# Kernel optimization log

Measured on AMD Instinct MI355X. Metric: run time of the kernel, lower is better.

## Reference

```python
import jax, jax.numpy as jnp
import numpy as np

N, E, H, L, G = 20000, 320000, 256, 7, 512
ATOM_V, BOND_V, OUT = 128, 8, 128
EPS = 1e-7      # GENConv eps added after ReLU on messages
BN_EPS = 1e-5   # BatchNorm1d default eps


def setup_inputs() -> dict:
    key = jax.random.key(0)
    ks = jax.random.split(key, 9)
    return {
        "node_feats": jax.random.randint(ks[0], (N, 9), 0, 100, dtype=jnp.int32),
        "edge_feats": jax.random.randint(ks[1], (E, 3), 0, 5, dtype=jnp.int32),
        "src": jax.random.randint(ks[2], (E,), 0, N, dtype=jnp.int32),
        "dst": jax.random.randint(ks[3], (E,), 0, N, dtype=jnp.int32),
        "graph_ids": jnp.sort(jax.random.randint(ks[4], (N,), 0, G, dtype=jnp.int32)),
        "atom_emb": 0.1 * jax.random.normal(ks[5], (9, ATOM_V, H), dtype=jnp.float32),
        "bond_emb": 0.1 * jax.random.normal(ks[6], (L, 3, BOND_V, H), dtype=jnp.float32),
        "bn_gamma": jnp.ones((L, H), jnp.float32),
        "bn_beta": jnp.zeros((L, H), jnp.float32),
        "mlp_w": (1.0 / np.sqrt(H)) * jax.random.normal(ks[7], (L, H, H), dtype=jnp.float32),
        "mlp_b": jnp.zeros((L, H), jnp.float32),
        "w_out": (1.0 / np.sqrt(H)) * jax.random.normal(ks[8], (H, OUT), dtype=jnp.float32),
        "b_out": jnp.zeros((OUT,), jnp.float32),
    }


def reference(node_feats, edge_feats, src, dst, graph_ids,
              atom_emb, bond_emb, bn_gamma, bn_beta, mlp_w, mlp_b, w_out, b_out):
    # AtomEncoder: sum of per-column embeddings -> [N, H]
    hv = atom_emb[jnp.arange(9)[None, :], node_feats].sum(axis=1)
    col3 = jnp.arange(3)[None, :]
    for l in range(L):
        # BatchNorm1d (training-mode batch stats) -> ReLU  (dropout p=0)
        mu = hv.mean(axis=0)
        var = hv.var(axis=0)
        h1 = (hv - mu) * jax.lax.rsqrt(var + BN_EPS) * bn_gamma[l] + bn_beta[l]
        h1 = jax.nn.relu(h1)
        # GENConv: BondEncoder embedding, message = relu(h_src + he) + eps
        he = bond_emb[l][col3, edge_feats].sum(axis=1)          # [E, H]
        m = jax.nn.relu(h1[src] + he) + EPS                     # [E, H]
        # edge softmax over incoming edges per destination node (beta = 1.0)
        mmax = jax.ops.segment_max(m, dst, num_segments=N)      # [N, H]
        ex = jnp.exp(m - mmax[dst])
        denom = jax.ops.segment_sum(ex, dst, num_segments=N)    # [N, H]
        a = ex / denom[dst]
        agg = jax.ops.segment_sum(m * a, dst, num_segments=N)   # [N, H]
        # MLP (mlp_layers=1 -> single Linear) + outer residual
        hv = (h1 + agg) @ mlp_w[l] + mlp_b[l] + hv
    # AvgPooling over nodes of each graph
    cnt = jax.ops.segment_sum(jnp.ones((N,), hv.dtype), graph_ids, num_segments=G)
    hg = jax.ops.segment_sum(hv, graph_ids, num_segments=G) / jnp.maximum(cnt, 1.0)[:, None]
    return hg @ w_out + b_out  # [G, OUT]
```

## Files before the change

kernel.cpp:

```cpp
#include <hip/hip_runtime.h>

#define N_NODES 20000
#define N_EDGES 320000
#define HD 256
#define NLAYERS 7
#define NGRAPH 512
#define NOUT 128
#define NTILES 625

typedef __attribute__((ext_vector_type(8))) short bf16x8;
typedef __attribute__((ext_vector_type(4))) int i32x4;
typedef __attribute__((ext_vector_type(4))) float f32x4;

__device__ __forceinline__ ushort f2bf(float f) {
    union { float f; unsigned u; } v;
    v.f = f;
    unsigned r = (v.u + 0x7FFFu + ((v.u >> 16) & 1u)) >> 16;
    return (ushort)r;
}
__device__ __forceinline__ float bf2f(ushort u) {
    union { unsigned u; float f; } v;
    v.u = (unsigned)u << 16;
    return v.f;
}
__device__ __forceinline__ float bflo(unsigned p) {
    union { unsigned u; float f; } v;
    v.u = p << 16;
    return v.f;
}
__device__ __forceinline__ float bfhi(unsigned p) {
    union { unsigned u; float f; } v;
    v.u = p & 0xffff0000u;
    return v.f;
}

__global__ __launch_bounds__(256) void hist_kernel(const int* __restrict__ dst, int* __restrict__ hist) {
    int e = blockIdx.x * 256 + threadIdx.x;
    if (e < N_EDGES) atomicAdd(&hist[dst[e]], 1);
}

__global__ __launch_bounds__(1024) void scan_kernel(const int* __restrict__ hist,
                                                    int* __restrict__ row_ptr,
                                                    int* __restrict__ cursor) {
    __shared__ int sums[1024];
    int t = threadIdx.x;
    const int CH = 20;
    int base = t * CH;
    int local[20];
    int s = 0;
#pragma unroll
    for (int i = 0; i < CH; i++) {
        int v = (base + i < N_NODES) ? hist[base + i] : 0;
        local[i] = s;
        s += v;
    }
    sums[t] = s;
    __syncthreads();
    for (int off = 1; off < 1024; off <<= 1) {
        int v = (t >= off) ? sums[t - off] : 0;
        __syncthreads();
        sums[t] += v;
        __syncthreads();
    }
    int offset = (t == 0) ? 0 : sums[t - 1];
#pragma unroll
    for (int i = 0; i < CH; i++) {
        int idx = base + i;
        if (idx < N_NODES) {
            int v = offset + local[i];
            row_ptr[idx] = v;
            cursor[idx] = v;
        }
    }
    if (t == 1023) row_ptr[N_NODES] = sums[1023];
}

__global__ __launch_bounds__(256) void scatter_kernel(const int* __restrict__ dst,
                                                      const int* __restrict__ src,
                                                      const int* __restrict__ ef,
                                                      int* __restrict__ cursor,
                                                      unsigned* __restrict__ pack_sorted) {
    int e = blockIdx.x * 256 + threadIdx.x;
    if (e < N_EDGES) {
        int d = dst[e];
        int p = atomicAdd(&cursor[d], 1);
        unsigned cb = (unsigned)(ef[e * 3] * 25 + ef[e * 3 + 1] * 5 + ef[e * 3 + 2]);
        pack_sorted[p] = (unsigned)src[e] | (cb << 15);
    }
}

__global__ __launch_bounds__(256) void hetab_kernel(const float* __restrict__ bond,
                                                    ushort* __restrict__ he) {
    int idx = blockIdx.x * 256 + threadIdx.x;
    if (idx >= NLAYERS * 125 * HD) return;
    int h = idx & (HD - 1);
    int rem = idx >> 8;
    int l = rem / 125;
    int c = rem - l * 125;
    int f0 = c / 25, f1 = (c / 5) % 5, f2 = c % 5;
    const float* b = bond + (size_t)l * 3 * 8 * HD;
    he[idx] = f2bf(b[(0 * 8 + f0) * HD + h] + b[(1 * 8 + f1) * HD + h] + b[(2 * 8 + f2) * HD + h]);
}

__global__ __launch_bounds__(256) void wt_kernel(const float* __restrict__ W,
                                                 ushort* __restrict__ Wt) {
    int b = blockIdx.x;
    int l = b >> 8;
    int n = b & 255;
    int k = threadIdx.x;
    float v = W[((size_t)l * HD + k) * HD + n];
    int ks = k >> 5, kg = (k >> 3) & 3, j = k & 7;
    Wt[(((size_t)l * 8 + ks) * 256 + n) * 32 + kg * 8 + j] = f2bf(v);
}

__global__ __launch_bounds__(256) void atom_kernel(const int* __restrict__ nf,
                                                   const float* __restrict__ emb,
                                                   float* __restrict__ hv,
                                                   float* __restrict__ stats0) {
    int c = threadIdx.x;
    int n0 = blockIdx.x * 32;
    float s1 = 0.f, s2 = 0.f;
    for (int i = 0; i < 32; i++) {
        int n = n0 + i;
        const int* f = nf + n * 9;
        float v = 0.f;
#pragma unroll
        for (int j = 0; j < 9; j++) v += emb[(j * 128 + f[j]) * HD + c];
        hv[(size_t)n * HD + c] = v;
        s1 += v;
        s2 += v * v;
    }
    atomicAdd(&stats0[c], s1);
    atomicAdd(&stats0[HD + c], s2);
}

__global__ __launch_bounds__(256) void bn_kernel(const float* __restrict__ hv,
                                                 const float* __restrict__ stats,
                                                 const float* __restrict__ gamma,
                                                 const float* __restrict__ beta,
                                                 ushort* __restrict__ h1) {
    int tid = blockIdx.x * 256 + threadIdx.x;
    int idx = tid * 8;
    int c = idx & (HD - 1);
    float4 f0 = *reinterpret_cast<const float4*>(hv + idx);
    float4 f1 = *reinterpret_cast<const float4*>(hv + idx + 4);
    float v[8] = {f0.x, f0.y, f0.z, f0.w, f1.x, f1.y, f1.z, f1.w};
    ushort o[8];
#pragma unroll
    for (int j = 0; j < 8; j++) {
        float mu = stats[c + j] * (1.0f / N_NODES);
        float var = stats[HD + c + j] * (1.0f / N_NODES) - mu * mu;
        float a = gamma[c + j] * rsqrtf(fmaxf(var, 0.f) + 1e-5f);
        float b = beta[c + j] - mu * a;
        o[j] = f2bf(fmaxf(fmaf(v[j], a, b), 0.f));
    }
    i32x4 pack;
    pack.x = (int)o[0] | ((int)o[1] << 16);
    pack.y = (int)o[2] | ((int)o[3] << 16);
    pack.z = (int)o[4] | ((int)o[5] << 16);
    pack.w = (int)o[6] | ((int)o[7] << 16);
    *reinterpret_cast<i32x4*>(h1 + idx) = pack;
}

__global__ __launch_bounds__(256) void edge_kernel(const ushort* __restrict__ h1,
                                                   ushort* __restrict__ xbf,
                                                   const int* __restrict__ row_ptr,
                                                   const unsigned* __restrict__ pack_sorted,
                                                   const ushort* __restrict__ hetab) {
    int wv = threadIdx.x >> 6;
    int lane = threadIdx.x & 63;
    int n = blockIdx.x * 4 + wv;
    int c4 = lane * 4;
    int e0 = row_ptr[n];
    int deg = row_ptr[n + 1] - e0;

    float S0 = 0.f, S1 = 0.f, S2 = 0.f, S3 = 0.f;
    float T0 = 0.f, T1 = 0.f, T2 = 0.f, T3 = 0.f;

#define GATHER(i, P)                                                                          \
    uint2 hs##i = *reinterpret_cast<const uint2*>(h1 + ((size_t)((P) & 0x7FFFu) << 8) + c4);  \
    uint2 hb##i = *reinterpret_cast<const uint2*>(hetab + (((P) >> 15) << 8) + c4);

#define EDGE_PROC(HS, HB)                                                  \
    {                                                                      \
        float m0 = fmaxf(bflo(HS.x) + bflo(HB.x), 0.f);                    \
        float m1 = fmaxf(bfhi(HS.x) + bfhi(HB.x), 0.f);                    \
        float m2 = fmaxf(bflo(HS.y) + bflo(HB.y), 0.f);                    \
        float m3 = fmaxf(bfhi(HS.y) + bfhi(HB.y), 0.f);                    \
        float x0 = __expf(m0), x1 = __expf(m1), x2 = __expf(m2), x3 = __expf(m3); \
        S0 += x0; T0 = fmaf(m0, x0, T0);                                   \
        S1 += x1; T1 = fmaf(m1, x1, T1);                                   \
        S2 += x2; T2 = fmaf(m2, x2, T2);                                   \
        S3 += x3; T3 = fmaf(m3, x3, T3);                                   \
    }

    for (int base = 0; base < deg; base += 64) {
        int cnt = min(64, deg - base);
        unsigned pk = (lane < cnt) ? pack_sorted[e0 + base + lane] : 0u;
        int j = 0;
        for (; j + 4 <= cnt; j += 4) {
            unsigned p0 = __shfl(pk, j + 0);
            unsigned p1 = __shfl(pk, j + 1);
            unsigned p2 = __shfl(pk, j + 2);
            unsigned p3 = __shfl(pk, j + 3);
            GATHER(0, p0) GATHER(1, p1) GATHER(2, p2) GATHER(3, p3)
            EDGE_PROC(hs0, hb0) EDGE_PROC(hs1, hb1) EDGE_PROC(hs2, hb2) EDGE_PROC(hs3, hb3)
        }
        for (; j < cnt; j++) {
            unsigned p0 = __shfl(pk, j);
            GATHER(0, p0)
            EDGE_PROC(hs0, hb0)
        }
    }
#undef EDGE_PROC
#undef GATHER

    float a0 = (S0 > 0.f) ? (T0 / S0 + 1e-7f) : 0.f;
    float a1 = (S1 > 0.f) ? (T1 / S1 + 1e-7f) : 0.f;
    float a2 = (S2 > 0.f) ? (T2 / S2 + 1e-7f) : 0.f;
    float a3 = (S3 > 0.f) ? (T3 / S3 + 1e-7f) : 0.f;

    uint2 ho = *reinterpret_cast<const uint2*>(h1 + ((size_t)n << 8) + c4);
    unsigned o0 = f2bf(bflo(ho.x) + a0);
    unsigned o1 = f2bf(bfhi(ho.x) + a1);
    unsigned o2 = f2bf(bflo(ho.y) + a2);
    unsigned o3 = f2bf(bfhi(ho.y) + a3);
    uint2 res;
    res.x = o0 | (o1 << 16);
    res.y = o2 | (o3 << 16);
    *reinterpret_cast<uint2*>(xbf + ((size_t)n << 8) + c4) = res;
}

__global__ __launch_bounds__(256, 2) void mlp_mfma_kernel(const ushort* __restrict__ xbf,
                                                          float* __restrict__ hv,
                                                          const ushort* __restrict__ Wt,
                                                          const float* __restrict__ bias,
                                                          float* __restrict__ stats_next,
                                                          int accum_stats) {
    __shared__ __attribute__((aligned(16))) ushort xs[32 * 256];

    int t = threadIdx.x;
    int l = t & 63;
    int w = t >> 6;
    int kg = l >> 4;
    int lr = l & 15;

    const ushort* wbase = Wt + ((size_t)(w * 64 + lr)) * 32 + kg * 8;
    bf16x8 wreg[8][4];
#pragma unroll
    for (int ks = 0; ks < 8; ks++)
#pragma unroll
        for (int nt = 0; nt < 4; nt++)
            wreg[ks][nt] = *reinterpret_cast<const bf16x8*>(wbase + ks * 8192 + nt * 512);

    float bcol[4];
#pragma unroll
    for (int nt = 0; nt < 4; nt++) bcol[nt] = bias[w * 64 + nt * 16 + lr];

    float s1[4], s2[4];
#pragma unroll
    for (int nt = 0; nt < 4; nt++) { s1[nt] = 0.f; s2[nt] = 0.f; }

    for (int tile = blockIdx.x; tile < NTILES; tile += gridDim.x) {
        int row0 = tile * 32;
        const ushort* xbase = xbf + (size_t)row0 * HD;

        __syncthreads();
#pragma unroll
        for (int i = 0; i < 4; i++) {
            int flat = i * 2048 + t * 8;
            i32x4 iv = *reinterpret_cast<const i32x4*>(xbase + flat);
            int row = flat >> 8;
            int k8 = (flat >> 3) & 31;
            int sw = k8 ^ (row & 7);
            *reinterpret_cast<i32x4*>(&xs[row * 256 + sw * 8]) = iv;
        }
        __syncthreads();

        f32x4 acc[2][4];
#pragma unroll
        for (int m = 0; m < 2; m++)
#pragma unroll
            for (int n = 0; n < 4; n++) acc[m][n] = (f32x4){0.f, 0.f, 0.f, 0.f};

#define MFMASTEP(ks)                                                                             \
    {                                                                                            \
        int unit = (ks) * 4 + kg;                                                                \
        int rA0 = lr, rA1 = 16 + lr;                                                             \
        bf16x8 a0 = *reinterpret_cast<const bf16x8*>(&xs[rA0 * 256 + (unit ^ (rA0 & 7)) * 8]);   \
        bf16x8 a1 = *reinterpret_cast<const bf16x8*>(&xs[rA1 * 256 + (unit ^ (rA1 & 7)) * 8]);   \
        acc[0][0] = __builtin_amdgcn_mfma_f32_16x16x32_bf16(a0, wreg[ks][0], acc[0][0], 0, 0, 0);\
        acc[0][1] = __builtin_amdgcn_mfma_f32_16x16x32_bf16(a0, wreg[ks][1], acc[0][1], 0, 0, 0);\
        acc[0][2] = __builtin_amdgcn_mfma_f32_16x16x32_bf16(a0, wreg[ks][2], acc[0][2], 0, 0, 0);\
        acc[0][3] = __builtin_amdgcn_mfma_f32_16x16x32_bf16(a0, wreg[ks][3], acc[0][3], 0, 0, 0);\
        acc[1][0] = __builtin_amdgcn_mfma_f32_16x16x32_bf16(a1, wreg[ks][0], acc[1][0], 0, 0, 0);\
        acc[1][1] = __builtin_amdgcn_mfma_f32_16x16x32_bf16(a1, wreg[ks][1], acc[1][1], 0, 0, 0);\
        acc[1][2] = __builtin_amdgcn_mfma_f32_16x16x32_bf16(a1, wreg[ks][2], acc[1][2], 0, 0, 0);\
        acc[1][3] = __builtin_amdgcn_mfma_f32_16x16x32_bf16(a1, wreg[ks][3], acc[1][3], 0, 0, 0);\
    }
        MFMASTEP(0) MFMASTEP(1) MFMASTEP(2) MFMASTEP(3)
        MFMASTEP(4) MFMASTEP(5) MFMASTEP(6) MFMASTEP(7)
#undef MFMASTEP

#pragma unroll
        for (int mt = 0; mt < 2; mt++) {
#pragma unroll
            for (int r = 0; r < 4; r++) {
                size_t base = (size_t)(row0 + mt * 16 + kg * 4 + r) * HD;
#pragma unroll
                for (int nt = 0; nt < 4; nt++) {
                    int col = w * 64 + nt * 16 + lr;
                    float v = acc[mt][nt][r] + bcol[nt] + hv[base + col];
                    hv[base + col] = v;
                    s1[nt] += v;
                    s2[nt] += v * v;
                }
            }
        }
    }

    if (accum_stats) {
#pragma unroll
        for (int nt = 0; nt < 4; nt++) {
            s1[nt] += __shfl_xor(s1[nt], 16);
            s1[nt] += __shfl_xor(s1[nt], 32);
            s2[nt] += __shfl_xor(s2[nt], 16);
            s2[nt] += __shfl_xor(s2[nt], 32);
        }
        if (l < 16) {
#pragma unroll
            for (int nt = 0; nt < 4; nt++) {
                int col = w * 64 + nt * 16 + l;
                atomicAdd(&stats_next[col], s1[nt]);
                atomicAdd(&stats_next[HD + col], s2[nt]);
            }
        }
    }
}

__global__ __launch_bounds__(256) void pool_kernel(const float* __restrict__ hv,
                                                   const int* __restrict__ gid,
                                                   float* __restrict__ hg,
                                                   float* __restrict__ cnt) {
    int c = threadIdx.x;
    int n0 = blockIdx.x * 32;
    int curg = gid[n0];
    float s = 0.f;
    int runlen = 0;
    for (int i = 0; i < 32; i++) {
        int n = n0 + i;
        int g = gid[n];
        if (g != curg) {
            atomicAdd(&hg[curg * HD + c], s);
            if (c == 0) atomicAdd(&cnt[curg], (float)runlen);
            curg = g;
            s = 0.f;
            runlen = 0;
        }
        s += hv[(size_t)n * HD + c];
        runlen++;
    }
    atomicAdd(&hg[curg * HD + c], s);
    if (c == 0) atomicAdd(&cnt[curg], (float)runlen);
}

__global__ __launch_bounds__(128) void out_kernel(const float* __restrict__ hg,
                                                  const float* __restrict__ cnt,
                                                  const float* __restrict__ wout,
                                                  const float* __restrict__ bout,
                                                  float* __restrict__ out) {
    __shared__ float hr[HD];
    int g = blockIdx.x, o = threadIdx.x;
    float inv = 1.0f / fmaxf(cnt[g], 1.0f);
    hr[o] = hg[g * HD + o] * inv;
    hr[o + 128] = hg[g * HD + o + 128] * inv;
    __syncthreads();
    float acc = bout[o];
#pragma unroll 4
    for (int k = 0; k < HD; k++) acc = fmaf(hr[k], wout[k * NOUT + o], acc);
    out[g * NOUT + o] = acc;
}

extern "C" void kernel_launch(void* const* d_in, const int* in_sizes, int n_in,
                              void* d_out, int out_size, void* d_ws, size_t ws_size,
                              hipStream_t stream) {
    const int* node_feats = (const int*)d_in[0];
    const int* edge_feats = (const int*)d_in[1];
    const int* src = (const int*)d_in[2];
    const int* dst = (const int*)d_in[3];
    const int* gid = (const int*)d_in[4];
    const float* atom_emb = (const float*)d_in[5];
    const float* bond_emb = (const float*)d_in[6];
    const float* gamma = (const float*)d_in[7];
    const float* beta = (const float*)d_in[8];
    const float* mlp_w = (const float*)d_in[9];
    const float* mlp_b = (const float*)d_in[10];
    const float* w_out = (const float*)d_in[11];
    const float* b_out = (const float*)d_in[12];
    float* out = (float*)d_out;

    float* ws = (float*)d_ws;
    float* hv = ws;
    ushort* h1 = (ushort*)(hv + (size_t)N_NODES * HD);
    ushort* xbf = h1 + (size_t)N_NODES * HD;
    ushort* Wt = xbf + (size_t)N_NODES * HD;
    ushort* hetabs = Wt + (size_t)NLAYERS * HD * HD;
    int* row_ptr = (int*)(hetabs + NLAYERS * 125 * HD);
    int* cursor = row_ptr + (N_NODES + 1);
    unsigned* pack_sorted = (unsigned*)(cursor + N_NODES);
    int* hist = (int*)(pack_sorted + N_EDGES);
    float* stats = (float*)(hist + N_NODES);
    float* hg = stats + NLAYERS * 2 * HD;
    float* cnt = hg + NGRAPH * HD;

    size_t zero_bytes = (size_t)(N_NODES + NLAYERS * 2 * HD + NGRAPH * HD + NGRAPH) * 4;
    hipMemsetAsync(hist, 0, zero_bytes, stream);

    hist_kernel<<<(N_EDGES + 255) / 256, 256, 0, stream>>>(dst, hist);
    scan_kernel<<<1, 1024, 0, stream>>>(hist, row_ptr, cursor);
    scatter_kernel<<<(N_EDGES + 255) / 256, 256, 0, stream>>>(dst, src, edge_feats, cursor,
                                                              pack_sorted);
    hetab_kernel<<<(NLAYERS * 125 * HD + 255) / 256, 256, 0, stream>>>(bond_emb, hetabs);
    wt_kernel<<<NLAYERS * HD, 256, 0, stream>>>(mlp_w, Wt);
    atom_kernel<<<N_NODES / 32, 256, 0, stream>>>(node_feats, atom_emb, hv, stats);

    for (int l = 0; l < NLAYERS; l++) {
        bn_kernel<<<N_NODES * HD / 8 / 256, 256, 0, stream>>>(hv, stats + l * 2 * HD,
                                                              gamma + l * HD, beta + l * HD, h1);
        edge_kernel<<<N_NODES / 4, 256, 0, stream>>>(h1, xbf, row_ptr, pack_sorted,
                                                     hetabs + (size_t)l * 125 * HD);
        mlp_mfma_kernel<<<512, 256, 0, stream>>>(xbf, hv, Wt + (size_t)l * 8 * 256 * 32,
                                                 mlp_b + l * HD, stats + (l + 1) * 2 * HD,
                                                 (l < NLAYERS - 1) ? 1 : 0);
    }

    pool_kernel<<<N_NODES / 32, 256, 0, stream>>>(hv, gid, hg, cnt);
    out_kernel<<<NGRAPH, 128, 0, stream>>>(hg, cnt, w_out, b_out, out);
}
```

Baseline: 610.7 us.

## Stage bond-embedding table in LDS and use persistent half-wave-per-node edge kernel

The edge kernel now copies the per-layer 125x256 bf16 bond embedding table (about 64 KB) into shared memory once per block. It then loops persistently over nodes, with each 32-lane half-wave handling one node and 16-byte loads of 8 channels per lane. This removes the repeated global gathers of the bond table and widens the source-feature gathers. In exchange, the large LDS footprint limits occupancy, each block pays a 64 KB preload, and the fixed 512-block grid may load-balance uneven node degrees less well.

```diff
diff --git a/kernel.cpp b/kernel.cpp
--- a/kernel.cpp
+++ b/kernel.cpp
@@ -162,73 +162,95 @@
     *reinterpret_cast<i32x4*>(h1 + idx) = pack;
 }
 
-__global__ __launch_bounds__(256) void edge_kernel(const ushort* __restrict__ h1,
-                                                   ushort* __restrict__ xbf,
-                                                   const int* __restrict__ row_ptr,
-                                                   const unsigned* __restrict__ pack_sorted,
-                                                   const ushort* __restrict__ hetab) {
-    int wv = threadIdx.x >> 6;
-    int lane = threadIdx.x & 63;
-    int n = blockIdx.x * 4 + wv;
-    int c4 = lane * 4;
-    int e0 = row_ptr[n];
-    int deg = row_ptr[n + 1] - e0;
-
-    float S0 = 0.f, S1 = 0.f, S2 = 0.f, S3 = 0.f;
-    float T0 = 0.f, T1 = 0.f, T2 = 0.f, T3 = 0.f;
-
-#define GATHER(i, P)                                                                          \
-    uint2 hs##i = *reinterpret_cast<const uint2*>(h1 + ((size_t)((P) & 0x7FFFu) << 8) + c4);  \
-    uint2 hb##i = *reinterpret_cast<const uint2*>(hetab + (((P) >> 15) << 8) + c4);
-
-#define EDGE_PROC(HS, HB)                                                  \
-    {                                                                      \
-        float m0 = fmaxf(bflo(HS.x) + bflo(HB.x), 0.f);                    \
-        float m1 = fmaxf(bfhi(HS.x) + bfhi(HB.x), 0.f);                    \
-        float m2 = fmaxf(bflo(HS.y) + bflo(HB.y), 0.f);                    \
-        float m3 = fmaxf(bfhi(HS.y) + bfhi(HB.y), 0.f);                    \
+__global__ __launch_bounds__(256, 2) void edge_kernel(const ushort* __restrict__ h1,
+                                                      ushort* __restrict__ xbf,
+                                                      const int* __restrict__ row_ptr,
+                                                      const unsigned* __restrict__ pack_sorted,
+                                                      const ushort* __restrict__ hetab) {
+    __shared__ __attribute__((aligned(16))) ushort hetab_lds[125 * 256];
+    for (int i = threadIdx.x; i < 125 * 256 / 8; i += 256)
+        reinterpret_cast<uint4*>(hetab_lds)[i] = reinterpret_cast<const uint4*>(hetab)[i];
+    __syncthreads();
+
+    int half = threadIdx.x >> 5;
+    int lane = threadIdx.x & 31;
+    int c8 = lane * 8;
+
+#define PROC8(HS, HB)                                                       \
+    {                                                                       \
+        float m0 = fmaxf(bflo(HS.x) + bflo(HB.x), 0.f);                     \
+        float m1 = fmaxf(bfhi(HS.x) + bfhi(HB.x), 0.f);                     \
+        float m2 = fmaxf(bflo(HS.y) + bflo(HB.y), 0.f);                     \
+        float m3 = fmaxf(bfhi(HS.y) + bfhi(HB.y), 0.f);                     \
+        float m4 = fmaxf(bflo(HS.z) + bflo(HB.z), 0.f);                     \
+        float m5 = fmaxf(bfhi(HS.z) + bfhi(HB.z), 0.f);                     \
+        float m6 = fmaxf(bflo(HS.w) + bflo(HB.w), 0.f);                     \
+        float m7 = fmaxf(bfhi(HS.w) + bfhi(HB.w), 0.f);                     \
         float x0 = __expf(m0), x1 = __expf(m1), x2 = __expf(m2), x3 = __expf(m3); \
-        S0 += x0; T0 = fmaf(m0, x0, T0);                                   \
-        S1 += x1; T1 = fmaf(m1, x1, T1);                                   \
-        S2 += x2; T2 = fmaf(m2, x2, T2);                                   \
-        S3 += x3; T3 = fmaf(m3, x3, T3);                                   \
-    }
-
-    for (int base = 0; base < deg; base += 64) {
-        int cnt = min(64, deg - base);
-        unsigned pk = (lane < cnt) ? pack_sorted[e0 + base + lane] : 0u;
-        int j = 0;
-        for (; j + 4 <= cnt; j += 4) {
-            unsigned p0 = __shfl(pk, j + 0);
-            unsigned p1 = __shfl(pk, j + 1);
-            unsigned p2 = __shfl(pk, j + 2);
-            unsigned p3 = __shfl(pk, j + 3);
-            GATHER(0, p0) GATHER(1, p1) GATHER(2, p2) GATHER(3, p3)
-            EDGE_PROC(hs0, hb0) EDGE_PROC(hs1, hb1) EDGE_PROC(hs2, hb2) EDGE_PROC(hs3, hb3)
-        }
-        for (; j < cnt; j++) {
-            unsigned p0 = __shfl(pk, j);
-            GATHER(0, p0)
-            EDGE_PROC(hs0, hb0)
-        }
-    }
-#undef EDGE_PROC
-#undef GATHER
-
-    float a0 = (S0 > 0.f) ? (T0 / S0 + 1e-7f) : 0.f;
-    float a1 = (S1 > 0.f) ? (T1 / S1 + 1e-7f) : 0.f;
-    float a2 = (S2 > 0.f) ? (T2 / S2 + 1e-7f) : 0.f;
-    float a3 = (S3 > 0.f) ? (T3 / S3 + 1e-7f) : 0.f;
-
-    uint2 ho = *reinterpret_cast<const uint2*>(h1 + ((size_t)n << 8) + c4);
-    unsigned o0 = f2bf(bflo(ho.x) + a0);
-    unsigned o1 = f2bf(bfhi(ho.x) + a1);
-    unsigned o2 = f2bf(bflo(ho.y) + a2);
-    unsigned o3 = f2bf(bfhi(ho.y) + a3);
-    uint2 res;
-    res.x = o0 | (o1 << 16);
-    res.y = o2 | (o3 << 16);
-    *reinterpret_cast<uint2*>(xbf + ((size_t)n << 8) + c4) = res;
+        float x4 = __expf(m4), x5 = __expf(m5), x6 = __expf(m6), x7 = __expf(m7); \
+        S[0] += x0; T[0] = fmaf(m0, x0, T[0]);                              \
+        S[1] += x1; T[1] = fmaf(m1, x1, T[1]);                              \
+        S[2] += x2; T[2] = fmaf(m2, x2, T[2]);                              \
+        S[3] += x3; T[3] = fmaf(m3, x3, T[3]);                              \
+        S[4] += x4; T[4] = fmaf(m4, x4, T[4]);                              \
+        S[5] += x5; T[5] = fmaf(m5, x5, T[5]);                              \
+        S[6] += x6; T[6] = fmaf(m6, x6, T[6]);                              \
+        S[7] += x7; T[7] = fmaf(m7, x7, T[7]);                              \
+    }
+
+#define GATHER8(i, P)                                                                            \
+    uint4 hs##i = *reinterpret_cast<const uint4*>(h1 + ((size_t)((P) & 0x7FFFu) << 8) + c8);     \
+    uint4 hb##i = *reinterpret_cast<const uint4*>(&hetab_lds[((P) >> 15) * 256 + c8]);
+
+    for (int n = blockIdx.x * 8 + half; n < N_NODES; n += gridDim.x * 8) {
+        int e0 = row_ptr[n];
+        int deg = row_ptr[n + 1] - e0;
+
+        float S[8], T[8];
+#pragma unroll
+        for (int q = 0; q < 8; q++) { S[q] = 0.f; T[q] = 0.f; }
+
+        for (int base = 0; base < deg; base += 32) {
+            int cnt = min(32, deg - base);
+            unsigned pk = (lane < cnt) ? pack_sorted[e0 + base + lane] : 0u;
+            int j = 0;
+            for (; j + 4 <= cnt; j += 4) {
+                unsigned p0 = __shfl(pk, j + 0, 32);
+                unsigned p1 = __shfl(pk, j + 1, 32);
+                unsigned p2 = __shfl(pk, j + 2, 32);
+                unsigned p3 = __shfl(pk, j + 3, 32);
+                GATHER8(0, p0) GATHER8(1, p1) GATHER8(2, p2) GATHER8(3, p3)
+                PROC8(hs0, hb0) PROC8(hs1, hb1) PROC8(hs2, hb2) PROC8(hs3, hb3)
+            }
+            for (; j < cnt; j++) {
+                unsigned p0 = __shfl(pk, j, 32);
+                GATHER8(0, p0)
+                PROC8(hs0, hb0)
+            }
+        }
+
+        float a[8];
+#pragma unroll
+        for (int q = 0; q < 8; q++) a[q] = (S[q] > 0.f) ? (T[q] / S[q] + 1e-7f) : 0.f;
+
+        uint4 ho = *reinterpret_cast<const uint4*>(h1 + ((size_t)n << 8) + c8);
+        unsigned o0 = f2bf(bflo(ho.x) + a[0]);
+        unsigned o1 = f2bf(bfhi(ho.x) + a[1]);
+        unsigned o2 = f2bf(bflo(ho.y) + a[2]);
+        unsigned o3 = f2bf(bfhi(ho.y) + a[3]);
+        unsigned o4 = f2bf(bflo(ho.z) + a[4]);
+        unsigned o5 = f2bf(bfhi(ho.z) + a[5]);
+        unsigned o6 = f2bf(bflo(ho.w) + a[6]);
+        unsigned o7 = f2bf(bfhi(ho.w) + a[7]);
+        uint4 res;
+        res.x = o0 | (o1 << 16);
+        res.y = o2 | (o3 << 16);
+        res.z = o4 | (o5 << 16);
+        res.w = o6 | (o7 << 16);
+        *reinterpret_cast<uint4*>(xbf + ((size_t)n << 8) + c8) = res;
+    }
+#undef PROC8
+#undef GATHER8
 }
 
 __global__ __launch_bounds__(256, 2) void mlp_mfma_kernel(const ushort* __restrict__ xbf,
@@ -427,8 +449,8 @@
     for (int l = 0; l < NLAYERS; l++) {
         bn_kernel<<<N_NODES * HD / 8 / 256, 256, 0, stream>>>(hv, stats + l * 2 * HD,
                                                               gamma + l * HD, beta + l * HD, h1);
-        edge_kernel<<<N_NODES / 4, 256, 0, stream>>>(h1, xbf, row_ptr, pack_sorted,
-                                                     hetabs + (size_t)l * 125 * HD);
+        edge_kernel<<<512, 256, 0, stream>>>(h1, xbf, row_ptr, pack_sorted,
+                                             hetabs + (size_t)l * 125 * HD);
         mlp_mfma_kernel<<<512, 256, 0, stream>>>(xbf, hv, Wt + (size_t)l * 8 * 256 * 32,
                                                  mlp_b + l * HD, stats + (l + 1) * 2 * HD,
                                                  (l < NLAYERS - 1) ? 1 : 0);
```

New measurement: 728.9 us. +19.4%, slower.
